# Kernel optimization log

Hardware: AMD Instinct MI355X
Metric: run time of the kernel (lower is better)

Reference implementation:

```python
import jax, jax.numpy as jnp
import numpy as np

DECAY = 0.6
GAIN = 0.4


def _layernorm(x, g, b, eps=1e-5):
    m = x.mean(-1, keepdims=True)
    v = x.var(-1, keepdims=True)
    return (x - m) * jax.lax.rsqrt(v + eps) * g + b


def _ema_scan(x, axis, reverse=False):
    # linear recurrence state = 0.6*state + 0.4*x as an associative scan
    a = jnp.full_like(x, DECAY)
    b = GAIN * x
    def comb(c1, c2):
        a1, b1 = c1
        a2, b2 = c2
        return a1 * a2, a2 * b1 + b2
    _, y = jax.lax.associative_scan(comb, (a, b), axis=axis, reverse=reverse)
    return y


def setup_inputs() -> dict:
    key = jax.random.key(0)
    B, H, W, D = 16, 64, 64, 384
    inner = 2 * D
    hidden = 4 * D
    ks = jax.random.split(key, 12)
    s = 0.02
    return {
        "x": jax.random.normal(ks[0], (B, H, W, D), jnp.float32),
        "n1_g": jnp.ones((D,), jnp.float32),
        "n1_b": jnp.zeros((D,), jnp.float32),
        "w_in": s * jax.random.normal(ks[1], (D, inner), jnp.float32),
        "b_in": jnp.zeros((inner,), jnp.float32),
        "k_conv": s * jax.random.normal(ks[2], (3, 3, 1, inner), jnp.float32),  # depthwise HWIO
        "on_g": jnp.ones((inner,), jnp.float32),
        "on_b": jnp.zeros((inner,), jnp.float32),
        "w_out": s * jax.random.normal(ks[3], (inner, D), jnp.float32),
        "b_out": jnp.zeros((D,), jnp.float32),
        "n2_g": jnp.ones((D,), jnp.float32),
        "n2_b": jnp.zeros((D,), jnp.float32),
        "w1": s * jax.random.normal(ks[4], (D, hidden), jnp.float32),
        "b1": jnp.zeros((hidden,), jnp.float32),
        "w2": s * jax.random.normal(ks[5], (hidden, D), jnp.float32),
        "b2": jnp.zeros((D,), jnp.float32),
    }


def reference(x, n1_g, n1_b, w_in, b_in, k_conv, on_g, on_b, w_out, b_out,
              n2_g, n2_b, w1, b1, w2, b2):
    inner = w_in.shape[1]
    # --- LegacyScan2DOperator branch ---
    h = _layernorm(x, n1_g, n1_b)
    p = h @ w_in + b_in  # [B,H,W,inner]
    local = jax.lax.conv_general_dilated(
        p, k_conv, window_strides=(1, 1), padding="SAME",
        dimension_numbers=("NHWC", "HWIO", "NHWC"),
        feature_group_count=inner)
    lr = _ema_scan(local, axis=2)                 # left->right over W
    rl = _ema_scan(local, axis=2, reverse=True)   # right->left
    tb = _ema_scan(local, axis=1)                 # top->bottom over H
    bt = _ema_scan(local, axis=1, reverse=True)   # bottom->top
    mixed = 0.25 * (lr + rl + tb + bt) + local
    mixed = _layernorm(mixed, on_g, on_b)
    x = x + (mixed @ w_out + b_out)
    # --- MLP branch ---
    h2 = _layernorm(x, n2_g, n2_b)
    m = jax.nn.gelu(h2 @ w1 + b1, approximate=False) @ w2 + b2
    return x + m
```

## Files before the change

kernel.cpp:

```cpp
#include <hip/hip_runtime.h>
#include <math.h>


typedef __attribute__((ext_vector_type(8))) short bf16x8;
typedef __attribute__((ext_vector_type(4))) float f32x4;

#define T_TOKENS 65536
#define DMODEL 384
#define DINNER 768
#define DHIDDEN 1536

__device__ __forceinline__ float bf2f(unsigned short u) {
  unsigned int x = ((unsigned int)u) << 16;
  return __builtin_bit_cast(float, x);
}
__device__ __forceinline__ unsigned short f2bf(float f) {
  unsigned int x = __builtin_bit_cast(unsigned int, f);
  x += 0x7fffu + ((x >> 16) & 1u);
  return (unsigned short)(x >> 16);
}
__device__ __forceinline__ void unpack2(unsigned int u, float& lo, float& hi) {
  lo = __builtin_bit_cast(float, u << 16);
  hi = __builtin_bit_cast(float, u & 0xffff0000u);
}
__device__ __forceinline__ unsigned int pack2(float lo, float hi) {
  return (unsigned int)f2bf(lo) | ((unsigned int)f2bf(hi) << 16);
}

__device__ __forceinline__ void gload16(const void* g, void* l) {
  __builtin_amdgcn_global_load_lds(
      (const __attribute__((address_space(1))) void*)g,
      (__attribute__((address_space(3))) void*)l, 16, 0, 0);
}

__global__ __launch_bounds__(256) void ln_fused_f32_384(
    const float* __restrict__ in, const float* __restrict__ g,
    const float* __restrict__ b, unsigned short* __restrict__ out) {
  const int tok = blockIdx.x * 4 + (threadIdx.x >> 6);
  const int lane = threadIdx.x & 63;
  const float2* row = (const float2*)(in + (size_t)tok * 384);
  float2 v[3];
  float s = 0.f, ss = 0.f;
#pragma unroll
  for (int k = 0; k < 3; k++) {
    v[k] = row[lane + 64 * k];
    s += v[k].x + v[k].y;
    ss += v[k].x * v[k].x + v[k].y * v[k].y;
  }
#pragma unroll
  for (int off = 32; off > 0; off >>= 1) {
    s += __shfl_xor(s, off);
    ss += __shfl_xor(ss, off);
  }
  const float m = s * (1.0f / 384.0f);
  const float r = rsqrtf(ss * (1.0f / 384.0f) - m * m + 1e-5f);
  unsigned int* op = (unsigned int*)(out + (size_t)tok * 384);
#pragma unroll
  for (int k = 0; k < 3; k++) {
    const int c = lane + 64 * k;
    const float2 gg = ((const float2*)g)[c];
    const float2 bb = ((const float2*)b)[c];
    op[c] = pack2((v[k].x - m) * r * gg.x + bb.x, (v[k].y - m) * r * gg.y + bb.y);
  }
}

__global__ __launch_bounds__(256) void ln_fused_bf16_768(
    const unsigned short* __restrict__ in, const float* __restrict__ g,
    const float* __restrict__ b, unsigned short* __restrict__ out) {
  const int tok = blockIdx.x * 4 + (threadIdx.x >> 6);
  const int lane = threadIdx.x & 63;
  const uint2* row = (const uint2*)(in + (size_t)tok * 768);
  uint2 u[3];
  float s = 0.f, ss = 0.f;
  float e[3][4];
#pragma unroll
  for (int k = 0; k < 3; k++) {
    u[k] = row[lane + 64 * k];
    unpack2(u[k].x, e[k][0], e[k][1]);
    unpack2(u[k].y, e[k][2], e[k][3]);
#pragma unroll
    for (int j = 0; j < 4; j++) {
      s += e[k][j];
      ss += e[k][j] * e[k][j];
    }
  }
#pragma unroll
  for (int off = 32; off > 0; off >>= 1) {
    s += __shfl_xor(s, off);
    ss += __shfl_xor(ss, off);
  }
  const float m = s * (1.0f / 768.0f);
  const float r = rsqrtf(ss * (1.0f / 768.0f) - m * m + 1e-5f);
  uint2* op = (uint2*)(out + (size_t)tok * 768);
#pragma unroll
  for (int k = 0; k < 3; k++) {
    const int c = lane + 64 * k;
    const float4 gg = ((const float4*)g)[c];
    const float4 bb = ((const float4*)b)[c];
    uint2 w;
    w.x = pack2((e[k][0] - m) * r * gg.x + bb.x, (e[k][1] - m) * r * gg.y + bb.y);
    w.y = pack2((e[k][2] - m) * r * gg.z + bb.z, (e[k][3] - m) * r * gg.w + bb.w);
    op[c] = w;
  }
}

__global__ __launch_bounds__(256) void wprep_kernel(const float* __restrict__ in,
                                                    unsigned short* __restrict__ out,
                                                    int K, int N) {
  __shared__ float t[32][33];
  const int k0 = blockIdx.x * 32, n0 = blockIdx.y * 32;
  const int a = threadIdx.x & 31, b8 = threadIdx.x >> 5;
#pragma unroll
  for (int i = 0; i < 4; i++)
    t[b8 + 8 * i][a] = in[(size_t)(k0 + b8 + 8 * i) * N + n0 + a];
  __syncthreads();
#pragma unroll
  for (int i = 0; i < 4; i++)
    out[(size_t)(n0 + b8 + 8 * i) * K + k0 + a] = f2bf(t[a][b8 + 8 * i]);
}

template <int EPI>
__global__ __launch_bounds__(256) void gemm_bt_kernel(
    const unsigned short* __restrict__ A, int lda,
    const unsigned short* __restrict__ Bt, int ldb, int KT,
    const float* __restrict__ bias, const float* __restrict__ res,
    void* __restrict__ C, int ldc, int nby) {
  __shared__ unsigned short As[2][8192];
  __shared__ unsigned short Bs[2][8192];

  const int tid = threadIdx.x;
  const int w = tid >> 6, lane = tid & 63;
  const int cpx = gridDim.x >> 3;
  const int g = blockIdx.x;
  const int sw = (g & 7) * cpx + (g >> 3);
  const int bx = sw / nby, by = sw - bx * nby;
  const int tok0 = bx << 7, n0 = by << 7;

  const int wm = w >> 1, wn = w & 1;
  const int lrow = lane & 15, kgrp = lane >> 4;
  const int cx = lrow & 7;

  const int lr8 = lane >> 3;
  const int kce = ((lane & 7) ^ lr8) << 3;
  const unsigned short* Abase = A + (size_t)(tok0 + w * 32 + lr8) * lda + kce;
  const unsigned short* Bbase = Bt + (size_t)(n0 + w * 32 + lr8) * ldb + kce;

  f32x4 acc[4][4];
#pragma unroll
  for (int i = 0; i < 4; i++)
#pragma unroll
    for (int j = 0; j < 4; j++) {
      f32x4 z = {0.f, 0.f, 0.f, 0.f};
      acc[i][j] = z;
    }

  const int nt = KT >> 6;
#pragma unroll
  for (int i = 0; i < 4; i++) {
    gload16(Abase + (size_t)i * 8 * lda, (char*)As[0] + (w * 4 + i) * 1024);
    gload16(Bbase + (size_t)i * 8 * ldb, (char*)Bs[0] + (w * 4 + i) * 1024);
  }
  __syncthreads();

  int buf = 0;
  for (int t = 0; t < nt; t++) {
    if (t + 1 < nt) {
      const int kt = (t + 1) << 6;
#pragma unroll
      for (int i = 0; i < 4; i++) {
        gload16(Abase + (size_t)i * 8 * lda + kt,
                (char*)As[buf ^ 1] + (w * 4 + i) * 1024);
        gload16(Bbase + (size_t)i * 8 * ldb + kt,
                (char*)Bs[buf ^ 1] + (w * 4 + i) * 1024);
      }
    }
    bf16x8 af[2][4], bf_[2][4];
#pragma unroll
    for (int ks = 0; ks < 2; ks++) {
#pragma unroll
      for (int f = 0; f < 4; f++) {
        const int co = ((ks * 4 + kgrp) ^ cx) << 4;
        af[ks][f] = *(const bf16x8*)((const char*)As[buf] +
                                     (wm * 64 + f * 16 + lrow) * 128 + co);
        bf_[ks][f] = *(const bf16x8*)((const char*)Bs[buf] +
                                      (wn * 64 + f * 16 + lrow) * 128 + co);
      }
    }
#pragma unroll
    for (int ks = 0; ks < 2; ks++)
#pragma unroll
      for (int mf = 0; mf < 4; mf++)
#pragma unroll
        for (int nf = 0; nf < 4; nf++)
          acc[mf][nf] = __builtin_amdgcn_mfma_f32_16x16x32_bf16(
              af[ks][mf], bf_[ks][nf], acc[mf][nf], 0, 0, 0);
    __syncthreads();
    buf ^= 1;
  }

#pragma unroll
  for (int mf = 0; mf < 4; mf++) {
#pragma unroll
    for (int nf = 0; nf < 4; nf++) {
      const int gcol = n0 + wn * 64 + nf * 16 + lrow;
      const float bv = bias ? bias[gcol] : 0.0f;
#pragma unroll
      for (int r = 0; r < 4; r++) {
        const int grow = tok0 + wm * 64 + mf * 16 + kgrp * 4 + r;
        float v = acc[mf][nf][r] + bv;
        const size_t idx = (size_t)grow * ldc + gcol;
        if constexpr (EPI == 0) {
          ((unsigned short*)C)[idx] = f2bf(v);
        } else if constexpr (EPI == 1) {
          ((float*)C)[idx] = v + res[idx];
        } else {
          const float z = 1.5957691216057308f * (v + 0.044715f * v * v * v);
          const float gl = v / (1.0f + __expf(-z));
          ((unsigned short*)C)[idx] = f2bf(gl);
        }
      }
    }
  }
}

__global__ __launch_bounds__(256) void dwconv_kernel(
    const unsigned short* __restrict__ p, const float* __restrict__ kw,
    unsigned short* __restrict__ out) {
  const int u = blockIdx.x * 256 + threadIdx.x;
  const int cg = u % 96;
  const int pos = u / 96;
  const int c = cg * 8;
  const int w = pos & 63;
  const int h = (pos >> 6) & 63;
  const int b = pos >> 12;

  float acc[8];
#pragma unroll
  for (int j = 0; j < 8; j++) acc[j] = 0.f;

#pragma unroll
  for (int dh = 0; dh < 3; dh++) {
    const int hh = h + dh - 1;
    const bool vh = (unsigned)hh < 64u;
    const int hcl = min(max(hh, 0), 63);
    const size_t rb = ((size_t)((b << 12) + (hcl << 6))) * DINNER + c;
#pragma unroll
    for (int dw = 0; dw < 3; dw++) {
      const int ww = w + dw - 1;
      const bool vv = vh && ((unsigned)ww < 64u);
      const int wcl = min(max(ww, 0), 63);
      uint4 pv = *(const uint4*)(p + rb + (size_t)wcl * DINNER);
      if (!vv) { pv.x = 0; pv.y = 0; pv.z = 0; pv.w = 0; }
      const float4 k0 = *(const float4*)(kw + (dh * 3 + dw) * DINNER + c);
      const float4 k1 = *(const float4*)(kw + (dh * 3 + dw) * DINNER + c + 4);
      float lo, hi;
      unpack2(pv.x, lo, hi); acc[0] += lo * k0.x; acc[1] += hi * k0.y;
      unpack2(pv.y, lo, hi); acc[2] += lo * k0.z; acc[3] += hi * k0.w;
      unpack2(pv.z, lo, hi); acc[4] += lo * k1.x; acc[5] += hi * k1.y;
      unpack2(pv.w, lo, hi); acc[6] += lo * k1.z; acc[7] += hi * k1.w;
    }
  }
  uint4 st;
  st.x = pack2(acc[0], acc[1]);
  st.y = pack2(acc[2], acc[3]);
  st.z = pack2(acc[4], acc[5]);
  st.w = pack2(acc[6], acc[7]);
  *(uint4*)(out + (size_t)pos * DINNER + c) = st;
}

__global__ __launch_bounds__(128) void scan_w_kernel(
    const unsigned short* __restrict__ local, unsigned short* __restrict__ out1) {
  const int c2 = blockIdx.x * 128 + threadIdx.x;
  const int bh = blockIdx.y;
  const unsigned int* lp = (const unsigned int*)(local + (size_t)bh * 64 * DINNER) + c2;
  unsigned int* op = (unsigned int*)(out1 + (size_t)bh * 64 * DINNER) + c2;
  unsigned int v2[64], f2[64];
#pragma unroll
  for (int w = 0; w < 64; w++) v2[w] = lp[w * (DINNER / 2)];
  float ya = 0.f, yb = 0.f;
#pragma unroll
  for (int w = 0; w < 64; w++) {
    float a, b;
    unpack2(v2[w], a, b);
    ya = 0.6f * ya + 0.4f * a;
    yb = 0.6f * yb + 0.4f * b;
    f2[w] = pack2(ya, yb);
  }
  ya = 0.f; yb = 0.f;
#pragma unroll
  for (int w = 63; w >= 0; w--) {
    float a, b, fa, fb;
    unpack2(v2[w], a, b);
    ya = 0.6f * ya + 0.4f * a;
    yb = 0.6f * yb + 0.4f * b;
    unpack2(f2[w], fa, fb);
    op[w * (DINNER / 2)] = pack2(a + 0.25f * (fa + ya), b + 0.25f * (fb + yb));
  }
}

__global__ __launch_bounds__(128) void scan_h_kernel(
    const unsigned short* __restrict__ local, unsigned short* inout) {
  const int c2 = blockIdx.x * 128 + threadIdx.x;
  const int bw = blockIdx.y;
  const int b = bw >> 6, w = bw & 63;
  const unsigned int base = (unsigned int)(b * 4096 + w) * (DINNER / 2) + c2;
  const unsigned int sh = 64 * (DINNER / 2);
  const unsigned int* lp = (const unsigned int*)local + base;
  unsigned int* io = (unsigned int*)inout + base;
  unsigned int v2[64], f2[64];
#pragma unroll
  for (int h = 0; h < 64; h++) v2[h] = lp[h * sh];
  float ya = 0.f, yb = 0.f;
#pragma unroll
  for (int h = 0; h < 64; h++) {
    float a, b;
    unpack2(v2[h], a, b);
    ya = 0.6f * ya + 0.4f * a;
    yb = 0.6f * yb + 0.4f * b;
    f2[h] = pack2(ya, yb);
  }
  ya = 0.f; yb = 0.f;
#pragma unroll
  for (int h = 63; h >= 0; h--) {
    float a, b, fa, fb, oa, ob;
    unpack2(v2[h], a, b);
    ya = 0.6f * ya + 0.4f * a;
    yb = 0.6f * yb + 0.4f * b;
    unpack2(f2[h], fa, fb);
    unpack2(io[h * sh], oa, ob);
    io[h * sh] = pack2(oa + 0.25f * (fa + ya), ob + 0.25f * (fb + yb));
  }
}

extern "C" void kernel_launch(void* const* d_in, const int* in_sizes, int n_in,
                              void* d_out, int out_size, void* d_ws,
                              size_t ws_size, hipStream_t stream) {
  const float* x = (const float*)d_in[0];
  const float* n1_g = (const float*)d_in[1];
  const float* n1_b = (const float*)d_in[2];
  const float* w_in = (const float*)d_in[3];
  const float* b_in = (const float*)d_in[4];
  const float* k_conv = (const float*)d_in[5];
  const float* on_g = (const float*)d_in[6];
  const float* on_b = (const float*)d_in[7];
  const float* w_out = (const float*)d_in[8];
  const float* b_out = (const float*)d_in[9];
  const float* n2_g = (const float*)d_in[10];
  const float* n2_b = (const float*)d_in[11];
  const float* w1 = (const float*)d_in[12];
  const float* b1 = (const float*)d_in[13];
  const float* w2 = (const float*)d_in[14];
  const float* b2 = (const float*)d_in[15];

  const size_t MB = 1024 * 1024;
  char* ws = (char*)d_ws;
  unsigned short* R1 = (unsigned short*)(ws + 3 * MB / 2);
  unsigned short* R2 = (unsigned short*)(ws + 3 * MB / 2 + 96 * MB);

  unsigned short* A1 = R2;
  unsigned short* wTin = R2 + (48 * MB) / 2;
  unsigned short* p = R1;
  unsigned short* local = R2;
  unsigned short* mixed = R1;
  unsigned short* A2 = R2;
  unsigned short* wTout = R1;
  unsigned short* A3 = R1;
  unsigned short* wT1 = R1 + (48 * MB) / 2;
  unsigned short* wT2 = wT1 + (size_t)1536 * 384;
  unsigned short* gb = R2;

  float* out = (float*)d_out;
  dim3 b256(256);

  ln_fused_f32_384<<<T_TOKENS / 4, b256, 0, stream>>>(x, n1_g, n1_b, A1);
  wprep_kernel<<<dim3(12, 24), b256, 0, stream>>>(w_in, wTin, DMODEL, DINNER);
  gemm_bt_kernel<0><<<3072, b256, 0, stream>>>(A1, DMODEL, wTin, DMODEL, DMODEL,
                                               b_in, nullptr, p, DINNER, 6);
  dwconv_kernel<<<T_TOKENS * 96 / 256, b256, 0, stream>>>(p, k_conv, local);
  scan_w_kernel<<<dim3(3, 1024), dim3(128), 0, stream>>>(local, mixed);
  scan_h_kernel<<<dim3(3, 1024), dim3(128), 0, stream>>>(local, mixed);
  ln_fused_bf16_768<<<T_TOKENS / 4, b256, 0, stream>>>(mixed, on_g, on_b, A2);
  wprep_kernel<<<dim3(24, 12), b256, 0, stream>>>(w_out, wTout, DINNER, DMODEL);
  gemm_bt_kernel<1><<<1536, b256, 0, stream>>>(A2, DINNER, wTout, DINNER, DINNER,
                                               b_out, x, out, DMODEL, 3);
  ln_fused_f32_384<<<T_TOKENS / 4, b256, 0, stream>>>(out, n2_g, n2_b, A3);
  wprep_kernel<<<dim3(12, 48), b256, 0, stream>>>(w1, wT1, DMODEL, DHIDDEN);
  wprep_kernel<<<dim3(48, 12), b256, 0, stream>>>(w2, wT2, DHIDDEN, DMODEL);
  for (int hh = 0; hh < 2; hh++) {
    const size_t toff = (size_t)hh * 32768;
    gemm_bt_kernel<2><<<3072, b256, 0, stream>>>(
        A3 + toff * DMODEL, DMODEL, wT1, DMODEL, DMODEL, b1, nullptr, gb,
        DHIDDEN, 12);
    gemm_bt_kernel<1><<<768, b256, 0, stream>>>(
        gb, DHIDDEN, wT2, DHIDDEN, DHIDDEN, b2, out + toff * DMODEL,
        out + toff * DMODEL, DMODEL, 3);
  }
}
```

Baseline: 734.6 us.

## Fuse depthwise conv and four-direction EMA scans into one LDS-resident kernel

Replaces the separate depthwise-conv, W-scan and H-scan kernels with a single kernel. Each block owns one batch image and 8 channels, and computes the 3x3 conv into shared memory. It then runs the forward and backward scans along H and W from LDS and writes the mixed result back in place over p. This removes the intermediate `local` buffer and several full-tensor read/write passes through HBM. In exchange it uses about 68KB of LDS per block plus large per-thread register arrays, which limits occupancy. The global loads and stores are also strided across tokens rather than contiguous.

```diff
diff --git a/kernel.cpp b/kernel.cpp
--- a/kernel.cpp
+++ b/kernel.cpp
@@ -223,112 +223,129 @@
   }
 }
 
-__global__ __launch_bounds__(256) void dwconv_kernel(
-    const unsigned short* __restrict__ p, const float* __restrict__ kw,
-    unsigned short* __restrict__ out) {
-  const int u = blockIdx.x * 256 + threadIdx.x;
-  const int cg = u % 96;
-  const int pos = u / 96;
-  const int c = cg * 8;
-  const int w = pos & 63;
-  const int h = (pos >> 6) & 63;
-  const int b = pos >> 12;
-
-  float acc[8];
-#pragma unroll
-  for (int j = 0; j < 8; j++) acc[j] = 0.f;
-
-#pragma unroll
-  for (int dh = 0; dh < 3; dh++) {
-    const int hh = h + dh - 1;
-    const bool vh = (unsigned)hh < 64u;
-    const int hcl = min(max(hh, 0), 63);
-    const size_t rb = ((size_t)((b << 12) + (hcl << 6))) * DINNER + c;
-#pragma unroll
-    for (int dw = 0; dw < 3; dw++) {
-      const int ww = w + dw - 1;
-      const bool vv = vh && ((unsigned)ww < 64u);
-      const int wcl = min(max(ww, 0), 63);
-      uint4 pv = *(const uint4*)(p + rb + (size_t)wcl * DINNER);
-      if (!vv) { pv.x = 0; pv.y = 0; pv.z = 0; pv.w = 0; }
-      const float4 k0 = *(const float4*)(kw + (dh * 3 + dw) * DINNER + c);
-      const float4 k1 = *(const float4*)(kw + (dh * 3 + dw) * DINNER + c + 4);
-      float lo, hi;
-      unpack2(pv.x, lo, hi); acc[0] += lo * k0.x; acc[1] += hi * k0.y;
-      unpack2(pv.y, lo, hi); acc[2] += lo * k0.z; acc[3] += hi * k0.w;
-      unpack2(pv.z, lo, hi); acc[4] += lo * k1.x; acc[5] += hi * k1.y;
-      unpack2(pv.w, lo, hi); acc[6] += lo * k1.z; acc[7] += hi * k1.w;
-    }
-  }
-  uint4 st;
-  st.x = pack2(acc[0], acc[1]);
-  st.y = pack2(acc[2], acc[3]);
-  st.z = pack2(acc[4], acc[5]);
-  st.w = pack2(acc[6], acc[7]);
-  *(uint4*)(out + (size_t)pos * DINNER + c) = st;
-}
-
-__global__ __launch_bounds__(128) void scan_w_kernel(
-    const unsigned short* __restrict__ local, unsigned short* __restrict__ out1) {
-  const int c2 = blockIdx.x * 128 + threadIdx.x;
-  const int bh = blockIdx.y;
-  const unsigned int* lp = (const unsigned int*)(local + (size_t)bh * 64 * DINNER) + c2;
-  unsigned int* op = (unsigned int*)(out1 + (size_t)bh * 64 * DINNER) + c2;
-  unsigned int v2[64], f2[64];
-#pragma unroll
-  for (int w = 0; w < 64; w++) v2[w] = lp[w * (DINNER / 2)];
-  float ya = 0.f, yb = 0.f;
-#pragma unroll
-  for (int w = 0; w < 64; w++) {
-    float a, b;
-    unpack2(v2[w], a, b);
-    ya = 0.6f * ya + 0.4f * a;
-    yb = 0.6f * yb + 0.4f * b;
-    f2[w] = pack2(ya, yb);
-  }
-  ya = 0.f; yb = 0.f;
-#pragma unroll
-  for (int w = 63; w >= 0; w--) {
-    float a, b, fa, fb;
-    unpack2(v2[w], a, b);
-    ya = 0.6f * ya + 0.4f * a;
-    yb = 0.6f * yb + 0.4f * b;
-    unpack2(f2[w], fa, fb);
-    op[w * (DINNER / 2)] = pack2(a + 0.25f * (fa + ya), b + 0.25f * (fb + yb));
-  }
-}
-
-__global__ __launch_bounds__(128) void scan_h_kernel(
-    const unsigned short* __restrict__ local, unsigned short* inout) {
-  const int c2 = blockIdx.x * 128 + threadIdx.x;
-  const int bw = blockIdx.y;
-  const int b = bw >> 6, w = bw & 63;
-  const unsigned int base = (unsigned int)(b * 4096 + w) * (DINNER / 2) + c2;
-  const unsigned int sh = 64 * (DINNER / 2);
-  const unsigned int* lp = (const unsigned int*)local + base;
-  unsigned int* io = (unsigned int*)inout + base;
-  unsigned int v2[64], f2[64];
-#pragma unroll
-  for (int h = 0; h < 64; h++) v2[h] = lp[h * sh];
-  float ya = 0.f, yb = 0.f;
+__global__ __launch_bounds__(256) void conv_scan_kernel(
+    const unsigned int* __restrict__ p, const float* __restrict__ kconv,
+    unsigned int* __restrict__ mixed) {
+  __shared__ unsigned int loc[4][64][67];
+  const int tid = threadIdx.x;
+  const int cg = blockIdx.x;
+  const int b = blockIdx.y;
+  const int c4 = cg * 4;
+
+  float kw[9][8];
+#pragma unroll
+  for (int t = 0; t < 9; t++) {
+    const float4 ka = *(const float4*)(kconv + t * DINNER + c4 * 2);
+    const float4 kb = *(const float4*)(kconv + t * DINNER + c4 * 2 + 4);
+    kw[t][0] = ka.x; kw[t][1] = ka.y; kw[t][2] = ka.z; kw[t][3] = ka.w;
+    kw[t][4] = kb.x; kw[t][5] = kb.y; kw[t][6] = kb.z; kw[t][7] = kb.w;
+  }
+
+  const unsigned int* pb = p + (size_t)b * 4096 * (DINNER / 2) + c4;
+#pragma unroll 1
+  for (int i = 0; i < 16; i++) {
+    const int pos = tid + 256 * i;
+    const int h = pos >> 6, w = pos & 63;
+    float acc[8];
+#pragma unroll
+    for (int j = 0; j < 8; j++) acc[j] = 0.f;
+#pragma unroll
+    for (int dh = 0; dh < 3; dh++) {
+      const int hh = h + dh - 1;
+      const bool vh = (unsigned)hh < 64u;
+      const int hcl = min(max(hh, 0), 63);
+#pragma unroll
+      for (int dw = 0; dw < 3; dw++) {
+        const int ww = w + dw - 1;
+        const bool vv = vh && ((unsigned)ww < 64u);
+        const int wcl = min(max(ww, 0), 63);
+        uint4 pv = *(const uint4*)(pb + (size_t)(hcl * 64 + wcl) * (DINNER / 2));
+        if (!vv) { pv.x = 0; pv.y = 0; pv.z = 0; pv.w = 0; }
+        const int t = dh * 3 + dw;
+        float lo, hi;
+        unpack2(pv.x, lo, hi); acc[0] += lo * kw[t][0]; acc[1] += hi * kw[t][1];
+        unpack2(pv.y, lo, hi); acc[2] += lo * kw[t][2]; acc[3] += hi * kw[t][3];
+        unpack2(pv.z, lo, hi); acc[4] += lo * kw[t][4]; acc[5] += hi * kw[t][5];
+        unpack2(pv.w, lo, hi); acc[6] += lo * kw[t][6]; acc[7] += hi * kw[t][7];
+      }
+    }
+    loc[0][h][w] = pack2(acc[0], acc[1]);
+    loc[1][h][w] = pack2(acc[2], acc[3]);
+    loc[2][h][w] = pack2(acc[4], acc[5]);
+    loc[3][h][w] = pack2(acc[6], acc[7]);
+  }
+  __syncthreads();
+
+  const int ax = tid & 63;
+  const int cp = tid >> 6;
+
+  unsigned int hc[64];
+  {
+    float ya = 0.f, yb = 0.f;
+#pragma unroll
+    for (int h = 0; h < 64; h++) {
+      float a, bv;
+      unpack2(loc[cp][h][ax], a, bv);
+      ya = 0.6f * ya + 0.4f * a;
+      yb = 0.6f * yb + 0.4f * bv;
+      hc[h] = pack2(ya, yb);
+    }
+    ya = 0.f; yb = 0.f;
+#pragma unroll
+    for (int h = 63; h >= 0; h--) {
+      float a, bv, fa, fb;
+      unpack2(loc[cp][h][ax], a, bv);
+      ya = 0.6f * ya + 0.4f * a;
+      yb = 0.6f * yb + 0.4f * bv;
+      unpack2(hc[h], fa, fb);
+      hc[h] = pack2(0.25f * (fa + ya), 0.25f * (fb + yb));
+    }
+  }
+  unsigned int wt[64];
+  {
+    float ya = 0.f, yb = 0.f;
+#pragma unroll
+    for (int w = 0; w < 64; w++) {
+      float a, bv;
+      unpack2(loc[cp][ax][w], a, bv);
+      ya = 0.6f * ya + 0.4f * a;
+      yb = 0.6f * yb + 0.4f * bv;
+      wt[w] = pack2(ya, yb);
+    }
+    ya = 0.f; yb = 0.f;
+#pragma unroll
+    for (int w = 63; w >= 0; w--) {
+      float a, bv, fa, fb;
+      unpack2(loc[cp][ax][w], a, bv);
+      ya = 0.6f * ya + 0.4f * a;
+      yb = 0.6f * yb + 0.4f * bv;
+      unpack2(wt[w], fa, fb);
+      wt[w] = pack2(a + 0.25f * (fa + ya), bv + 0.25f * (fb + yb));
+    }
+  }
+  __syncthreads();
+#pragma unroll
+  for (int w = 0; w < 64; w++) loc[cp][ax][w] = wt[w];
+  __syncthreads();
 #pragma unroll
   for (int h = 0; h < 64; h++) {
-    float a, b;
-    unpack2(v2[h], a, b);
-    ya = 0.6f * ya + 0.4f * a;
-    yb = 0.6f * yb + 0.4f * b;
-    f2[h] = pack2(ya, yb);
-  }
-  ya = 0.f; yb = 0.f;
-#pragma unroll
-  for (int h = 63; h >= 0; h--) {
-    float a, b, fa, fb, oa, ob;
-    unpack2(v2[h], a, b);
-    ya = 0.6f * ya + 0.4f * a;
-    yb = 0.6f * yb + 0.4f * b;
-    unpack2(f2[h], fa, fb);
-    unpack2(io[h * sh], oa, ob);
-    io[h * sh] = pack2(oa + 0.25f * (fa + ya), ob + 0.25f * (fb + yb));
+    float a, bv, ca, cb;
+    unpack2(loc[cp][h][ax], a, bv);
+    unpack2(hc[h], ca, cb);
+    loc[cp][h][ax] = pack2(a + ca, bv + cb);
+  }
+  __syncthreads();
+  unsigned int* mb = mixed + (size_t)b * 4096 * (DINNER / 2) + c4;
+#pragma unroll 1
+  for (int i = 0; i < 16; i++) {
+    const int pos = tid + 256 * i;
+    const int h = pos >> 6, w = pos & 63;
+    uint4 st;
+    st.x = loc[0][h][w];
+    st.y = loc[1][h][w];
+    st.z = loc[2][h][w];
+    st.w = loc[3][h][w];
+    *(uint4*)(mb + (size_t)pos * (DINNER / 2)) = st;
   }
 }
 
@@ -360,8 +377,6 @@
   unsigned short* A1 = R2;
   unsigned short* wTin = R2 + (48 * MB) / 2;
   unsigned short* p = R1;
-  unsigned short* local = R2;
-  unsigned short* mixed = R1;
   unsigned short* A2 = R2;
   unsigned short* wTout = R1;
   unsigned short* A3 = R1;
@@ -376,10 +391,9 @@
   wprep_kernel<<<dim3(12, 24), b256, 0, stream>>>(w_in, wTin, DMODEL, DINNER);
   gemm_bt_kernel<0><<<3072, b256, 0, stream>>>(A1, DMODEL, wTin, DMODEL, DMODEL,
                                                b_in, nullptr, p, DINNER, 6);
-  dwconv_kernel<<<T_TOKENS * 96 / 256, b256, 0, stream>>>(p, k_conv, local);
-  scan_w_kernel<<<dim3(3, 1024), dim3(128), 0, stream>>>(local, mixed);
-  scan_h_kernel<<<dim3(3, 1024), dim3(128), 0, stream>>>(local, mixed);
-  ln_fused_bf16_768<<<T_TOKENS / 4, b256, 0, stream>>>(mixed, on_g, on_b, A2);
+  conv_scan_kernel<<<dim3(96, 16), b256, 0, stream>>>(
+      (const unsigned int*)p, k_conv, (unsigned int*)p);
+  ln_fused_bf16_768<<<T_TOKENS / 4, b256, 0, stream>>>(p, on_g, on_b, A2);
   wprep_kernel<<<dim3(24, 12), b256, 0, stream>>>(w_out, wTout, DINNER, DMODEL);
   gemm_bt_kernel<1><<<1536, b256, 0, stream>>>(A2, DINNER, wTout, DINNER, DINNER,
                                                b_out, x, out, DMODEL, 3);
```

Result: slower. 964.5 us (+31.3%).
